# Kernel tuning notes

Measured on AMD Instinct MI355X. Metric: run time of the kernel, lower is better.

## Reference

```python
import jax, jax.numpy as jnp
import numpy as np

D_MODEL, D_FF, N_EXPERTS, TOP_K = 1024, 4096, 8, 2

def setup_inputs() -> dict:
    key = jax.random.key(0)
    k1, k2, k3, k4 = jax.random.split(key, 4)
    x = jax.random.normal(k1, (4, 2048, D_MODEL), dtype=jnp.float32)
    # glorot-ish scaled init for weights
    router = jax.random.normal(k2, (D_MODEL, N_EXPERTS), dtype=jnp.float32) * (1.0 / np.sqrt(D_MODEL))
    W1 = jax.random.normal(k3, (N_EXPERTS, D_MODEL, D_FF), dtype=jnp.float32) * (1.0 / np.sqrt(D_MODEL))
    W2 = jax.random.normal(k4, (N_EXPERTS, D_FF, D_MODEL), dtype=jnp.float32) * (1.0 / np.sqrt(D_FF))
    return {"x": x, "router": router, "W1": W1, "W2": W2}

def reference(x, router, W1, W2):
    B, S, d = x.shape
    E = router.shape[1]
    xf = x.reshape(-1, d)                              # [T, d]
    logits = xf @ router                               # [T, E]
    top_v, top_i = jax.lax.top_k(logits, TOP_K)        # [T, k]
    w = jax.nn.softmax(top_v, axis=-1)                 # softmax over selected experts
    # scatter top-k weights into a dense [T, E] gate matrix (indices are distinct)
    gates = jnp.sum(jax.nn.one_hot(top_i, E, dtype=x.dtype) * w[..., None], axis=1)
    out = jnp.zeros_like(xf)
    for e in range(E):                                 # small fixed expert loop
        h = xf @ W1[e]                                 # [T, d_ff]
        h = h * jax.nn.sigmoid(h)                      # swish
        out = out + gates[:, e:e + 1] * (h @ W2[e])    # weighted combine
    return out.reshape(B, S, d)
```

## Files before the change

kernel.cpp:

```cpp
#include <hip/hip_runtime.h>
#include <hip/hip_bf16.h>

#define NTOK 8192
#define DM 1024
#define DFF 4096
#define NE 8
#define TPAD 72

typedef __attribute__((ext_vector_type(8))) short bf16x8;
typedef __attribute__((ext_vector_type(4))) float f32x4;

__device__ __forceinline__ ushort f2bf(float f) {
  __hip_bfloat16 h = __float2bfloat16(f);
  return *reinterpret_cast<ushort*>(&h);
}

template <int K, int N>
__global__ void pack_w(const float* __restrict__ in, ushort* __restrict__ outp) {
  __shared__ float t[64][129];
  const int e = blockIdx.z, nT = blockIdx.x, kt = blockIdx.y;
  const float* src = in + (size_t)e * K * N + (size_t)kt * 64 * N + (size_t)nT * 128;
  const int tid = threadIdx.x;
#pragma unroll
  for (int it = 0; it < 8; ++it) {
    int idx = it * 256 + tid;
    int kl = idx >> 5, n4 = idx & 31;
    f32x4 v = __builtin_nontemporal_load(
        reinterpret_cast<const f32x4*>(src + (size_t)kl * N + n4 * 4));
    t[kl][n4 * 4 + 0] = v.x; t[kl][n4 * 4 + 1] = v.y;
    t[kl][n4 * 4 + 2] = v.z; t[kl][n4 * 4 + 3] = v.w;
  }
  __syncthreads();
  const int row = tid >> 1, half = tid & 1;
  const int s = (row & 7) << 3;
  union { ushort us[32]; uint4 q[4]; } u;
#pragma unroll
  for (int k2 = 0; k2 < 32; ++k2) u.us[k2] = f2bf(t[(half * 32 + k2) ^ s][row]);
  ushort* dst = outp + ((size_t)(e * (N / 128) + nT) * (K / 64) + kt) * 8192 + row * 64 + half * 32;
  uint4* d4 = reinterpret_cast<uint4*>(dst);
  d4[0] = u.q[0]; d4[1] = u.q[1]; d4[2] = u.q[2]; d4[3] = u.q[3];
}

__global__ void router_kernel(const float* __restrict__ x, const float* __restrict__ router,
                              int* __restrict__ cnt, int* __restrict__ list,
                              float* __restrict__ wa, ushort* __restrict__ xb) {
  __shared__ float rl[DM * NE];
  int tid = threadIdx.x;
  for (int i = tid; i < DM * NE / 4; i += 256)
    reinterpret_cast<float4*>(rl)[i] = reinterpret_cast<const float4*>(router)[i];
  __syncthreads();
  int wave = tid >> 6, lane = tid & 63;
  int tok0 = blockIdx.x * 32 + wave * 8;
  for (int tI = 0; tI < 8; ++tI) {
    int tok = tok0 + tI;
    float acc[NE];
#pragma unroll
    for (int e2 = 0; e2 < NE; ++e2) acc[e2] = 0.f;
    const float4* xr = reinterpret_cast<const float4*>(x + (size_t)tok * DM);
    ushort xo[16];
#pragma unroll
    for (int c = 0; c < 4; ++c) {
      float4 v = xr[lane * 4 + c];
      int d = lane * 16 + c * 4;
      const float* vv = reinterpret_cast<const float*>(&v);
#pragma unroll
      for (int q = 0; q < 4; ++q) {
        float xv = vv[q];
        xo[c * 4 + q] = f2bf(xv);
#pragma unroll
        for (int e2 = 0; e2 < NE; ++e2) acc[e2] += xv * rl[(d + q) * NE + e2];
      }
    }
    *reinterpret_cast<uint4*>(xb + (size_t)tok * DM + lane * 16) =
        *reinterpret_cast<const uint4*>(&xo[0]);
    *reinterpret_cast<uint4*>(xb + (size_t)tok * DM + lane * 16 + 8) =
        *reinterpret_cast<const uint4*>(&xo[8]);
    for (int off = 32; off > 0; off >>= 1) {
#pragma unroll
      for (int e2 = 0; e2 < NE; ++e2) acc[e2] += __shfl_xor(acc[e2], off, 64);
    }
    if (lane == 0) {
      int i0 = 0; float v0 = acc[0];
#pragma unroll
      for (int e2 = 1; e2 < NE; ++e2) { if (acc[e2] > v0) { v0 = acc[e2]; i0 = e2; } }
      int i1 = -1; float v1 = -3.4e38f;
#pragma unroll
      for (int e2 = 0; e2 < NE; ++e2) { if (e2 != i0 && acc[e2] > v1) { v1 = acc[e2]; i1 = e2; } }
      float e1 = expf(v1 - v0);
      float w0 = 1.f / (1.f + e1);
      float w1 = e1 / (1.f + e1);
      int s0 = atomicAdd(&cnt[i0], 1);
      list[i0 * NTOK + s0] = tok * 2;
      wa[tok * 2] = w0;
      int s1 = atomicAdd(&cnt[i1], 1);
      list[i1 * NTOK + s1] = tok * 2 + 1;
      wa[tok * 2 + 1] = w1;
    }
  }
}

__global__ void build_tiles(const int* __restrict__ cnt, unsigned* __restrict__ table) {
  if (threadIdx.x == 0) {
    int t = 0;
    for (int e = 0; e < NE; ++e) {
      int nt = (cnt[e] + 255) >> 8;
      for (int i = 0; i < nt; ++i) table[t++] = ((unsigned)e << 16) | (unsigned)i;
    }
    for (; t < TPAD; ++t) table[t] = 0xFFFFFFFFu;
  }
}

__device__ __forceinline__ void gl_lds16(unsigned long long g, void* s) {
  __builtin_amdgcn_global_load_lds(
      (const __attribute__((address_space(1))) unsigned int*)g,
      (__attribute__((address_space(3))) unsigned int*)s, 16, 0, 0);
}

#define WAITV0() asm volatile("s_waitcnt vmcnt(0)" ::: "memory")

__device__ __forceinline__ void BARRIER() {
  asm volatile("" ::: "memory");
  __builtin_amdgcn_s_barrier();
  asm volatile("" ::: "memory");
}

template <int PASS>
__launch_bounds__(1024, 4)
__global__ void moe_gemm(const ushort* __restrict__ Xb,
                         const ushort* __restrict__ Wp,
                         ushort* __restrict__ Hp,
                         const int* __restrict__ cnt,
                         const int* __restrict__ list,
                         const unsigned* __restrict__ table,
                         const float* __restrict__ wa,
                         float* __restrict__ out) {
  constexpr int NK = (PASS == 1) ? 16 : 32;

  const int bid = blockIdx.x;
  const int xcd = bid & 7;
  const int j = bid >> 3;
  int t, nTile, kc;
  if (PASS == 1) { t = j % TPAD; nTile = xcd * 2 + j / TPAD; kc = 0; }
  else           { t = j; nTile = xcd >> 1; kc = xcd & 1; }
  unsigned td = table[t];
  if (td == 0xFFFFFFFFu) return;
  const int e = td >> 16;
  const int tTile = td & 0xFFFF;
  const int n = cnt[e];

  __shared__ __attribute__((aligned(16))) char As[2][32768];
  __shared__ __attribute__((aligned(16))) char Bs[2][32768];
  __shared__ int aL[256];
  __shared__ unsigned long long pL[256];

  const int tid = threadIdx.x;
  if (tid < 256) {
    int slot = tTile * 256 + tid;
    int sl = (slot < n) ? slot : (n - 1);
    int a = list[e * NTOK + sl];
    if constexpr (PASS == 2) aL[tid] = (slot < n) ? a : -1;
    if constexpr (PASS == 1)
      pL[tid] = (unsigned long long)(Xb + (size_t)(a >> 1) * DM);
  }
  __syncthreads();

  const int sr = tid >> 3;
  const int sc = (tid & 7) * 16;
  const unsigned dOff = (unsigned)(sr * 128 + sc);
  unsigned long long sA0[2];
  if constexpr (PASS == 1) {
#pragma unroll
    for (int jj = 0; jj < 2; ++jj) {
      int row = jj * 128 + sr;
      sA0[jj] = pL[row] + (unsigned)(sc ^ ((row & 7) << 4));
    }
  } else {
    const char* Asrc = (const char*)Hp + ((size_t)t * 64 + kc * 32) * 32768;
#pragma unroll
    for (int jj = 0; jj < 2; ++jj)
      sA0[jj] = (unsigned long long)(Asrc + jj * 16384 + dOff);
  }
  unsigned long long sB0[2];
#pragma unroll
  for (int p = 0; p < 2; ++p) {
    size_t chunk = (PASS == 1) ? ((size_t)(e * 32 + nTile * 2 + p) * 16)
                               : ((size_t)(e * 8 + nTile * 2 + p) * 64 + kc * 32);
    sB0[p] = (unsigned long long)((const char*)Wp + chunk * 16384 + dOff);
  }

  const int wv = tid >> 6, lane = tid & 63;
  const int wm = wv >> 2, wn = wv & 3;

  f32x4 acc[4][4];
#pragma unroll
  for (int m = 0; m < 4; ++m)
#pragma unroll
    for (int nn = 0; nn < 4; ++nn) acc[m][nn] = (f32x4){0.f, 0.f, 0.f, 0.f};

  auto STAGE = [&](int b, int kt) {
    if constexpr (PASS == 1) {
#pragma unroll
      for (int jj = 0; jj < 2; ++jj)
        gl_lds16(sA0[jj] + (unsigned)kt * 128, As[b] + jj * 16384 + dOff);
    } else {
#pragma unroll
      for (int jj = 0; jj < 2; ++jj)
        gl_lds16(sA0[jj] + (unsigned)kt * 32768, As[b] + jj * 16384 + dOff);
    }
#pragma unroll
    for (int p = 0; p < 2; ++p)
      gl_lds16(sB0[p] + (unsigned)kt * 16384, Bs[b] + p * 16384 + dOff);
  };

  auto COMPUTE = [&](int b) {
#pragma unroll
    for (int kk = 0; kk < 2; ++kk) {
      const int kb = kk * 64 + (lane >> 4) * 16;
      bf16x8 af[4], bq[4];
#pragma unroll
      for (int m = 0; m < 4; ++m) {
        int row = wm * 64 + m * 16 + (lane & 15);
        af[m] = *reinterpret_cast<const bf16x8*>(As[b] + row * 128 + (kb ^ ((row & 7) << 4)));
      }
#pragma unroll
      for (int nn = 0; nn < 4; ++nn) {
        int row = wn * 64 + nn * 16 + (lane & 15);
        bq[nn] = *reinterpret_cast<const bf16x8*>(Bs[b] + row * 128 + (kb ^ ((row & 7) << 4)));
      }
      __builtin_amdgcn_s_setprio(1);
#pragma unroll
      for (int m = 0; m < 4; ++m)
#pragma unroll
        for (int nn = 0; nn < 4; ++nn)
          acc[m][nn] = __builtin_amdgcn_mfma_f32_16x16x32_bf16(af[m], bq[nn], acc[m][nn], 0, 0, 0);
      __builtin_amdgcn_s_setprio(0);
    }
  };

  STAGE(0, 0);
  WAITV0();
  BARRIER();
  int b = 0;
  for (int kt = 0; kt < NK; ++kt) {
    if (kt + 1 < NK) STAGE(b ^ 1, kt + 1);
    COMPUTE(b);
    WAITV0();
    BARRIER();
    b ^= 1;
  }

#pragma unroll
  for (int m = 0; m < 4; ++m) {
#pragma unroll
    for (int jr = 0; jr < 4; ++jr) {
      int lr = wm * 64 + m * 16 + (lane >> 4) * 4 + jr;
      if constexpr (PASS == 1) {
#pragma unroll
        for (int nn = 0; nn < 4; ++nn) {
          int cg = nTile * 256 + wn * 64 + nn * 16 + (lane & 15);
          float v = acc[m][nn][jr];
          size_t us = ((size_t)t * 64 + (cg >> 6)) * 16384 + (size_t)lr * 64 +
                      ((cg & 63) ^ ((lr & 7) << 3));
          Hp[us] = f2bf(v / (1.f + expf(-v)));
        }
      } else {
        int a = aL[lr];
        if (a < 0) continue;
        float w = wa[a];
        int tok = a >> 1;
        float* orow = out + (size_t)tok * DM + nTile * 256 + wn * 64 + (lane & 15);
#pragma unroll
        for (int nn = 0; nn < 4; ++nn)
          atomicAdd(&orow[nn * 16], w * acc[m][nn][jr]);
      }
    }
  }
}

extern "C" void kernel_launch(void* const* d_in, const int* in_sizes, int n_in,
                              void* d_out, int out_size, void* d_ws, size_t ws_size,
                              hipStream_t stream) {
  const float* x = (const float*)d_in[0];
  const float* router = (const float*)d_in[1];
  const float* W1 = (const float*)d_in[2];
  const float* W2 = (const float*)d_in[3];
  float* out = (float*)d_out;
  char* ws = (char*)d_ws;

  ushort* Xb  = (ushort*)(ws + 0);
  ushort* Wp1 = (ushort*)(ws + (size_t)16 * 1024 * 1024);
  ushort* Wp2 = (ushort*)(ws + 0);
  size_t off = (size_t)80 * 1024 * 1024;
  ushort* Hp = (ushort*)(ws + off); off += (size_t)TPAD * 64 * 32768;
  int* cnt  = (int*)(ws + off); off += 256;
  int* list = (int*)(ws + off); off += (size_t)NE * NTOK * 4;
  float* wa = (float*)(ws + off); off += (size_t)NTOK * 2 * 4;
  unsigned* table = (unsigned*)(ws + off); off += TPAD * 4;

  hipMemsetAsync(out, 0, (size_t)NTOK * DM * sizeof(float), stream);
  hipMemsetAsync(cnt, 0, NE * sizeof(int), stream);

  pack_w<DM, DFF><<<dim3(DFF / 128, DM / 64, NE), 256, 0, stream>>>(W1, Wp1);
  router_kernel<<<NTOK / 32, 256, 0, stream>>>(x, router, cnt, list, wa, Xb);
  build_tiles<<<1, 64, 0, stream>>>(cnt, table);

  moe_gemm<1><<<8 * 2 * TPAD, 1024, 0, stream>>>(Xb, Wp1, Hp, cnt, list, table, wa, out);

  pack_w<DFF, DM><<<dim3(DM / 128, DFF / 64, NE), 256, 0, stream>>>(W2, Wp2);

  moe_gemm<2><<<8 * TPAD, 1024, 0, stream>>>(Xb, Wp2, Hp, cnt, list, table, wa, out);
}
```

Measured before the change: 749.8 us.

## Switch MoE GEMM to 512-thread blocks with 4-stage K=32 LDS pipeline

The grouped GEMM now runs 8 waves of 512 threads, each computing 128x64 of the 256x256 tile, instead of 16 waves. The K step drops from 64 to 32, and LDS becomes a 4-slot ring buffer with three tiles in flight. Partial vmcnt waits and A/B loads interleaved between the two MFMA halves are meant to hide global-load latency better than the old double buffer with a full wait. Weight packing and the H layout change to 32-wide K chunks with a new swizzle to match. This adds accumulator register pressure (32 f32x4 per lane) and doubles the number of barriers per tile.

```diff
diff --git a/kernel.cpp b/kernel.cpp
--- a/kernel.cpp
+++ b/kernel.cpp
@@ -17,28 +17,31 @@
 
 template <int K, int N>
 __global__ void pack_w(const float* __restrict__ in, ushort* __restrict__ outp) {
-  __shared__ float t[64][129];
-  const int e = blockIdx.z, nT = blockIdx.x, kt = blockIdx.y;
-  const float* src = in + (size_t)e * K * N + (size_t)kt * 64 * N + (size_t)nT * 128;
+  __shared__ float t[64][257];
+  const int e = blockIdx.z, nT = blockIdx.x, k64 = blockIdx.y;
+  const float* src = in + (size_t)e * K * N + (size_t)k64 * 64 * N + (size_t)nT * 256;
   const int tid = threadIdx.x;
 #pragma unroll
-  for (int it = 0; it < 8; ++it) {
+  for (int it = 0; it < 16; ++it) {
     int idx = it * 256 + tid;
-    int kl = idx >> 5, n4 = idx & 31;
-    f32x4 v = __builtin_nontemporal_load(
-        reinterpret_cast<const f32x4*>(src + (size_t)kl * N + n4 * 4));
+    int kl = idx >> 6, n4 = idx & 63;
+    float4 v = *reinterpret_cast<const float4*>(src + (size_t)kl * N + n4 * 4);
     t[kl][n4 * 4 + 0] = v.x; t[kl][n4 * 4 + 1] = v.y;
     t[kl][n4 * 4 + 2] = v.z; t[kl][n4 * 4 + 3] = v.w;
   }
   __syncthreads();
-  const int row = tid >> 1, half = tid & 1;
-  const int s = (row & 7) << 3;
-  union { ushort us[32]; uint4 q[4]; } u;
-#pragma unroll
-  for (int k2 = 0; k2 < 32; ++k2) u.us[k2] = f2bf(t[(half * 32 + k2) ^ s][row]);
-  ushort* dst = outp + ((size_t)(e * (N / 128) + nT) * (K / 64) + kt) * 8192 + row * 64 + half * 32;
-  uint4* d4 = reinterpret_cast<uint4*>(dst);
-  d4[0] = u.q[0]; d4[1] = u.q[1]; d4[2] = u.q[2]; d4[3] = u.q[3];
+  const int r = tid;
+  const int swap = (r & 6) << 2;
+#pragma unroll
+  for (int s = 0; s < 2; ++s) {
+    union { ushort us[32]; uint4 q[4]; } u;
+#pragma unroll
+    for (int j = 0; j < 32; ++j) u.us[j ^ swap] = f2bf(t[s * 32 + j][r]);
+    ushort* dst = outp +
+        ((size_t)(e * (N / 256) + nT) * (K / 32) + (k64 * 2 + s)) * 8192 + r * 32;
+    uint4* d4 = reinterpret_cast<uint4*>(dst);
+    d4[0] = u.q[0]; d4[1] = u.q[1]; d4[2] = u.q[2]; d4[3] = u.q[3];
+  }
 }
 
 __global__ void router_kernel(const float* __restrict__ x, const float* __restrict__ router,
@@ -116,7 +119,7 @@
       (__attribute__((address_space(3))) unsigned int*)s, 16, 0, 0);
 }
 
-#define WAITV0() asm volatile("s_waitcnt vmcnt(0)" ::: "memory")
+#define WAITV(N) asm volatile("s_waitcnt vmcnt(" #N ")" ::: "memory")
 
 __device__ __forceinline__ void BARRIER() {
   asm volatile("" ::: "memory");
@@ -125,7 +128,7 @@
 }
 
 template <int PASS>
-__launch_bounds__(1024, 4)
+__launch_bounds__(512, 2)
 __global__ void moe_gemm(const ushort* __restrict__ Xb,
                          const ushort* __restrict__ Wp,
                          ushort* __restrict__ Hp,
@@ -134,7 +137,7 @@
                          const unsigned* __restrict__ table,
                          const float* __restrict__ wa,
                          float* __restrict__ out) {
-  constexpr int NK = (PASS == 1) ? 16 : 32;
+  constexpr int NK = (PASS == 1) ? 32 : 64;
 
   const int bid = blockIdx.x;
   const int xcd = bid & 7;
@@ -148,8 +151,8 @@
   const int tTile = td & 0xFFFF;
   const int n = cnt[e];
 
-  __shared__ __attribute__((aligned(16))) char As[2][32768];
-  __shared__ __attribute__((aligned(16))) char Bs[2][32768];
+  __shared__ __attribute__((aligned(16))) char AsB[4 * 16384];
+  __shared__ __attribute__((aligned(16))) char BsB[4 * 16384];
   __shared__ int aL[256];
   __shared__ unsigned long long pL[256];
 
@@ -158,109 +161,110 @@
     int slot = tTile * 256 + tid;
     int sl = (slot < n) ? slot : (n - 1);
     int a = list[e * NTOK + sl];
-    if constexpr (PASS == 2) aL[tid] = (slot < n) ? a : -1;
+    aL[tid] = (slot < n) ? a : -1;
     if constexpr (PASS == 1)
       pL[tid] = (unsigned long long)(Xb + (size_t)(a >> 1) * DM);
   }
   __syncthreads();
 
-  const int sr = tid >> 3;
-  const int sc = (tid & 7) * 16;
-  const unsigned dOff = (unsigned)(sr * 128 + sc);
-  unsigned long long sA0[2];
+  const int sr = tid >> 2;
+  const int sq = (tid & 3) * 16;
+  const unsigned swzc = (unsigned)(sq ^ ((sr & 6) << 3));
+  unsigned long long pA0, pA1;
   if constexpr (PASS == 1) {
-#pragma unroll
-    for (int jj = 0; jj < 2; ++jj) {
-      int row = jj * 128 + sr;
-      sA0[jj] = pL[row] + (unsigned)(sc ^ ((row & 7) << 4));
-    }
+    pA0 = pL[sr] + swzc;
+    pA1 = pL[128 + sr] + (unsigned)(sq ^ (((128 + sr) & 6) << 3));
   } else {
-    const char* Asrc = (const char*)Hp + ((size_t)t * 64 + kc * 32) * 32768;
-#pragma unroll
-    for (int jj = 0; jj < 2; ++jj)
-      sA0[jj] = (unsigned long long)(Asrc + jj * 16384 + dOff);
-  }
-  unsigned long long sB0[2];
-#pragma unroll
-  for (int p = 0; p < 2; ++p) {
-    size_t chunk = (PASS == 1) ? ((size_t)(e * 32 + nTile * 2 + p) * 16)
-                               : ((size_t)(e * 8 + nTile * 2 + p) * 64 + kc * 32);
-    sB0[p] = (unsigned long long)((const char*)Wp + chunk * 16384 + dOff);
-  }
+    const char* Asrc = (const char*)Hp + ((size_t)t * 128 + kc * 64) * 16384;
+    pA0 = (unsigned long long)(Asrc + tid * 16);
+    pA1 = pA0 + 8192;
+  }
+  const size_t bChunk0 = (PASS == 1) ? ((size_t)(e * 16 + nTile) * 32)
+                                     : ((size_t)(e * 4 + nTile) * 128 + kc * 64);
+  const unsigned long long pB0 =
+      (unsigned long long)((const char*)Wp + bChunk0 * 16384 + tid * 16);
+  const unsigned dstOff = (unsigned)(tid * 16);
+
+  auto STG_A = [&](int s, int T) {
+    if constexpr (PASS == 1) {
+      gl_lds16(pA0 + (unsigned)T * 64, AsB + s * 16384 + dstOff);
+      gl_lds16(pA1 + (unsigned)T * 64, AsB + s * 16384 + 8192 + dstOff);
+    } else {
+      gl_lds16(pA0 + (unsigned)T * 16384, AsB + s * 16384 + dstOff);
+      gl_lds16(pA1 + (unsigned)T * 16384, AsB + s * 16384 + 8192 + dstOff);
+    }
+  };
+  auto STG_B = [&](int s, int T) {
+    gl_lds16(pB0 + (unsigned)T * 16384, BsB + s * 16384 + dstOff);
+    gl_lds16(pB0 + (unsigned)T * 16384 + 8192, BsB + s * 16384 + 8192 + dstOff);
+  };
 
   const int wv = tid >> 6, lane = tid & 63;
   const int wm = wv >> 2, wn = wv & 3;
-
-  f32x4 acc[4][4];
-#pragma unroll
-  for (int m = 0; m < 4; ++m)
+  const int l15 = lane & 15;
+  const unsigned rswz = (unsigned)(((lane >> 4) * 16) ^ ((l15 & 6) << 3));
+  const unsigned aRow0 = (unsigned)(wm * 128 + l15);
+  const unsigned bRow0 = (unsigned)(wn * 64 + l15);
+
+  f32x4 acc[8][4];
+#pragma unroll
+  for (int m = 0; m < 8; ++m)
 #pragma unroll
     for (int nn = 0; nn < 4; ++nn) acc[m][nn] = (f32x4){0.f, 0.f, 0.f, 0.f};
 
-  auto STAGE = [&](int b, int kt) {
-    if constexpr (PASS == 1) {
-#pragma unroll
-      for (int jj = 0; jj < 2; ++jj)
-        gl_lds16(sA0[jj] + (unsigned)kt * 128, As[b] + jj * 16384 + dOff);
-    } else {
-#pragma unroll
-      for (int jj = 0; jj < 2; ++jj)
-        gl_lds16(sA0[jj] + (unsigned)kt * 32768, As[b] + jj * 16384 + dOff);
-    }
-#pragma unroll
-    for (int p = 0; p < 2; ++p)
-      gl_lds16(sB0[p] + (unsigned)kt * 16384, Bs[b] + p * 16384 + dOff);
-  };
-
-  auto COMPUTE = [&](int b) {
-#pragma unroll
-    for (int kk = 0; kk < 2; ++kk) {
-      const int kb = kk * 64 + (lane >> 4) * 16;
-      bf16x8 af[4], bq[4];
-#pragma unroll
-      for (int m = 0; m < 4; ++m) {
-        int row = wm * 64 + m * 16 + (lane & 15);
-        af[m] = *reinterpret_cast<const bf16x8*>(As[b] + row * 128 + (kb ^ ((row & 7) << 4)));
-      }
-#pragma unroll
-      for (int nn = 0; nn < 4; ++nn) {
-        int row = wn * 64 + nn * 16 + (lane & 15);
-        bq[nn] = *reinterpret_cast<const bf16x8*>(Bs[b] + row * 128 + (kb ^ ((row & 7) << 4)));
-      }
-      __builtin_amdgcn_s_setprio(1);
-#pragma unroll
-      for (int m = 0; m < 4; ++m)
-#pragma unroll
-        for (int nn = 0; nn < 4; ++nn)
-          acc[m][nn] = __builtin_amdgcn_mfma_f32_16x16x32_bf16(af[m], bq[nn], acc[m][nn], 0, 0, 0);
-      __builtin_amdgcn_s_setprio(0);
-    }
-  };
-
-  STAGE(0, 0);
-  WAITV0();
-  BARRIER();
-  int b = 0;
-  for (int kt = 0; kt < NK; ++kt) {
-    if (kt + 1 < NK) STAGE(b ^ 1, kt + 1);
-    COMPUTE(b);
-    WAITV0();
+  STG_A(0, 0); STG_B(0, 0);
+  STG_A(1, 1); STG_B(1, 1);
+  STG_A(2, 2); STG_B(2, 2);
+
+  for (int T = 0; T < NK; ++T) {
+    const int sT = T & 3;
+    const int sN = (T + 3) & 3;
+    const char* a_ = AsB + sT * 16384;
+    const char* b_ = BsB + sT * 16384;
+    if (T < NK - 2) { WAITV(8); }
+    else if (T == NK - 2) { WAITV(4); }
+    else { WAITV(0); }
     BARRIER();
-    b ^= 1;
-  }
-
-#pragma unroll
-  for (int m = 0; m < 4; ++m) {
+    bf16x8 bq[4], af[4];
+#pragma unroll
+    for (int nn = 0; nn < 4; ++nn)
+      bq[nn] = *reinterpret_cast<const bf16x8*>(b_ + (bRow0 + nn * 16) * 64 + rswz);
+#pragma unroll
+    for (int m = 0; m < 4; ++m)
+      af[m] = *reinterpret_cast<const bf16x8*>(a_ + (aRow0 + m * 16) * 64 + rswz);
+    if (T + 3 < NK) STG_A(sN, T + 3);
+    __builtin_amdgcn_s_setprio(1);
+#pragma unroll
+    for (int m = 0; m < 4; ++m)
+#pragma unroll
+      for (int nn = 0; nn < 4; ++nn)
+        acc[m][nn] = __builtin_amdgcn_mfma_f32_16x16x32_bf16(af[m], bq[nn], acc[m][nn], 0, 0, 0);
+    __builtin_amdgcn_s_setprio(0);
+#pragma unroll
+    for (int m = 0; m < 4; ++m)
+      af[m] = *reinterpret_cast<const bf16x8*>(a_ + (aRow0 + 64 + m * 16) * 64 + rswz);
+    if (T + 3 < NK) STG_B(sN, T + 3);
+    __builtin_amdgcn_s_setprio(1);
+#pragma unroll
+    for (int m = 0; m < 4; ++m)
+#pragma unroll
+      for (int nn = 0; nn < 4; ++nn)
+        acc[4 + m][nn] = __builtin_amdgcn_mfma_f32_16x16x32_bf16(af[m], bq[nn], acc[4 + m][nn], 0, 0, 0);
+    __builtin_amdgcn_s_setprio(0);
+  }
+
+#pragma unroll
+  for (int m = 0; m < 8; ++m) {
 #pragma unroll
     for (int jr = 0; jr < 4; ++jr) {
-      int lr = wm * 64 + m * 16 + (lane >> 4) * 4 + jr;
+      int lr = wm * 128 + m * 16 + (lane >> 4) * 4 + jr;
       if constexpr (PASS == 1) {
+        int sw = (lr & 6) << 2;
 #pragma unroll
         for (int nn = 0; nn < 4; ++nn) {
-          int cg = nTile * 256 + wn * 64 + nn * 16 + (lane & 15);
+          int cg = nTile * 256 + wn * 64 + nn * 16 + l15;
           float v = acc[m][nn][jr];
-          size_t us = ((size_t)t * 64 + (cg >> 6)) * 16384 + (size_t)lr * 64 +
-                      ((cg & 63) ^ ((lr & 7) << 3));
+          size_t us = ((size_t)t * 128 + (cg >> 5)) * 8192 + (size_t)lr * 32 + ((cg & 31) ^ sw);
           Hp[us] = f2bf(v / (1.f + expf(-v)));
         }
       } else {
@@ -268,7 +272,7 @@
         if (a < 0) continue;
         float w = wa[a];
         int tok = a >> 1;
-        float* orow = out + (size_t)tok * DM + nTile * 256 + wn * 64 + (lane & 15);
+        float* orow = out + (size_t)tok * DM + nTile * 256 + wn * 64 + l15;
 #pragma unroll
         for (int nn = 0; nn < 4; ++nn)
           atomicAdd(&orow[nn * 16], w * acc[m][nn][jr]);
@@ -291,7 +295,7 @@
   ushort* Wp1 = (ushort*)(ws + (size_t)16 * 1024 * 1024);
   ushort* Wp2 = (ushort*)(ws + 0);
   size_t off = (size_t)80 * 1024 * 1024;
-  ushort* Hp = (ushort*)(ws + off); off += (size_t)TPAD * 64 * 32768;
+  ushort* Hp = (ushort*)(ws + off); off += (size_t)TPAD * 128 * 16384;
   int* cnt  = (int*)(ws + off); off += 256;
   int* list = (int*)(ws + off); off += (size_t)NE * NTOK * 4;
   float* wa = (float*)(ws + off); off += (size_t)NTOK * 2 * 4;
@@ -300,13 +304,13 @@
   hipMemsetAsync(out, 0, (size_t)NTOK * DM * sizeof(float), stream);
   hipMemsetAsync(cnt, 0, NE * sizeof(int), stream);
 
-  pack_w<DM, DFF><<<dim3(DFF / 128, DM / 64, NE), 256, 0, stream>>>(W1, Wp1);
+  pack_w<DM, DFF><<<dim3(DFF / 256, DM / 64, NE), 256, 0, stream>>>(W1, Wp1);
   router_kernel<<<NTOK / 32, 256, 0, stream>>>(x, router, cnt, list, wa, Xb);
   build_tiles<<<1, 64, 0, stream>>>(cnt, table);
 
-  moe_gemm<1><<<8 * 2 * TPAD, 1024, 0, stream>>>(Xb, Wp1, Hp, cnt, list, table, wa, out);
-
-  pack_w<DFF, DM><<<dim3(DM / 128, DFF / 64, NE), 256, 0, stream>>>(W2, Wp2);
-
-  moe_gemm<2><<<8 * TPAD, 1024, 0, stream>>>(Xb, Wp2, Hp, cnt, list, table, wa, out);
-}
+  moe_gemm<1><<<8 * 2 * TPAD, 512, 0, stream>>>(Xb, Wp1, Hp, cnt, list, table, wa, out);
+
+  pack_w<DFF, DM><<<dim3(DM / 256, DFF / 64, NE), 256, 0, stream>>>(W2, Wp2);
+
+  moe_gemm<2><<<8 * TPAD, 512, 0, stream>>>(Xb, Wp2, Hp, cnt, list, table, wa, out);
+}
```

After: 857.5 us. 14.4% more time.
